# Kernel tuning notes

Measured on AMD Instinct MI355X. Metric: run time of the kernel, lower is better.

The kernel has to match this reference:

```python
import jax, jax.numpy as jnp
import numpy as np

N = 32          # objects in the (single) image
P = N * (N - 1) # relation pairs
D = 256         # self.dim
M = 14          # mask_size / pooler resolution
OC = 151        # obj classes
RC = 51         # rel classes
RED = D // 4    # attention gate reduction


def setup_inputs() -> dict:
    key = jax.random.key(0)
    ks = jax.random.split(key, 32)
    # all ordered pairs i != j
    ii, jj = np.meshgrid(np.arange(N), np.arange(N), indexing='ij')
    keep = ii != jj
    rel_pair_idxs = jnp.asarray(np.stack([ii[keep], jj[keep]], 1), jnp.int32)  # [P,2]
    # valid xyxy boxes in an 800x600 image
    x1 = jax.random.uniform(ks[0], (N,)) * 600.0
    y1 = jax.random.uniform(ks[1], (N,)) * 400.0
    w = jax.random.uniform(ks[2], (N,)) * 180.0 + 20.0
    h = jax.random.uniform(ks[3], (N,)) * 180.0 + 20.0
    bboxes = jnp.stack([x1, y1, x1 + w, y1 + h], 1).astype(jnp.float32)
    roi_features = jax.random.normal(ks[4], (N, 4096), jnp.float32)
    predict_logits = jax.random.normal(ks[5], (N, OC), jnp.float32)
    union_features = jax.random.normal(ks[6], (P, D, M, M), jnp.float32)
    s = 0.02
    p = dict(
        roi_features=roi_features, bboxes=bboxes, predict_logits=predict_logits,
        union_features=union_features, rel_pair_idxs=rel_pair_idxs,
        W_emb1=jax.random.normal(ks[7], (4096 + OC + 4, D)) * s, b_emb1=jnp.zeros((D,)),
        W_emb2=jax.random.normal(ks[8], (D, D)) * s, b_emb2=jnp.zeros((D,)),
        # stacked SE-attention gates: 0=sbj, 1=obj, 2=bg
        att_fc1_w=jax.random.normal(ks[9], (3, D, RED)) * s, att_fc1_b=jnp.zeros((3, RED)),
        att_fc2_w=jax.random.normal(ks[10], (3, RED, D)) * s, att_fc2_b=jnp.zeros((3, D)),
        W_c1=jax.random.normal(ks[11], (3 * D, D)) * s, b_c1=jnp.zeros((D,)),
        W_c2=jax.random.normal(ks[12], (D, D)) * s, b_c2=jnp.zeros((D,)),
        W_gcn=jax.random.normal(ks[13], (D, D)) * s, b_gcn=jnp.zeros((D,)),
        W_objp=jax.random.normal(ks[14], (D, OC)) * s, b_objp=jnp.zeros((OC,)),
        W_relp=jax.random.normal(ks[15], (D, RC)) * s, b_relp=jnp.zeros((RC,)),
    )
    return p


def _rect_masks(x0, y0, x1, y1):
    # mask[p, r, c] = 1 iff x0<=r<x1 and y0<=c<y1  (matches torch slice write)
    r = jnp.arange(M, dtype=jnp.float32)
    rm = (r[None, :] >= x0[:, None]) & (r[None, :] < x1[:, None])  # [P,M]
    cm = (r[None, :] >= y0[:, None]) & (r[None, :] < y1[:, None])  # [P,M]
    return (rm[:, :, None] & cm[:, None, :]).astype(jnp.float32)   # [P,M,M]


def _masking(union_features, bboxes, pairs):
    sb = bboxes[pairs[:, 0]]  # [P,4]
    ob = bboxes[pairs[:, 1]]
    ux1 = jnp.minimum(sb[:, 0], ob[:, 0])
    uy1 = jnp.minimum(sb[:, 1], ob[:, 1])
    x = jnp.stack([sb[:, 0], sb[:, 2], ob[:, 0], ob[:, 2]], 1) - ux1[:, None]
    y = jnp.stack([sb[:, 1], sb[:, 3], ob[:, 1], ob[:, 3]], 1) - uy1[:, None]
    xr = M / jnp.maximum(x[:, 1], x[:, 3])
    yr = M / jnp.maximum(y[:, 1], y[:, 3])
    xp = jnp.round(x * xr[:, None])
    yp = jnp.round(y * yr[:, None])
    sm = _rect_masks(xp[:, 0], yp[:, 0], xp[:, 1], yp[:, 1])[:, None]  # [P,1,M,M]
    om = _rect_masks(xp[:, 2], yp[:, 2], xp[:, 3], yp[:, 3])[:, None]
    bm = jnp.clip(1.0 - sm - om, 0.0, 1.0)
    return union_features * sm, union_features * om, union_features * bm


def _att_gate(x, w1, b1, w2, b2):
    # SE-style channel attention gate
    s = x.mean((2, 3))                                        # [P,D]
    g = jax.nn.sigmoid(jax.nn.relu(s @ w1 + b1) @ w2 + b2)    # [P,D]
    return x * g[:, :, None, None]


def _adjacency(pairs):
    o2o = jnp.zeros((N, N)).at[pairs[:, 0], pairs[:, 1]].set(1.0)
    ar = jnp.arange(P)
    o2r = jnp.zeros((N, P)).at[pairs[:, 0], ar].set(1.0).at[pairs[:, 1], ar].set(1.0)
    top = jnp.concatenate([o2o, o2r], 1)                     # [N, N+P]
    bot = jnp.concatenate([o2r.T, jnp.zeros((P, P))], 1)     # [P, N+P]
    adj = jnp.concatenate([top, bot], 0)
    return adj + jnp.eye(N + P)


def reference(roi_features, bboxes, predict_logits, union_features, rel_pair_idxs,
              W_emb1, b_emb1, W_emb2, b_emb2,
              att_fc1_w, att_fc1_b, att_fc2_w, att_fc2_b,
              W_c1, b_c1, W_c2, b_c2, W_gcn, b_gcn,
              W_objp, b_objp, W_relp, b_relp):
    pairs = rel_pair_idxs
    # object embedding
    obj_in = jnp.concatenate([roi_features, predict_logits, bboxes], 1)  # [N,4251]
    obj_feats = jax.nn.relu(obj_in @ W_emb1 + b_emb1) @ W_emb2 + b_emb2  # [N,D]
    # masking + attention gates + global avg pool
    sbj, obj, bg = _masking(union_features, bboxes, pairs)
    sbj = _att_gate(sbj, att_fc1_w[0], att_fc1_b[0], att_fc2_w[0], att_fc2_b[0]).mean((2, 3))
    obj = _att_gate(obj, att_fc1_w[1], att_fc1_b[1], att_fc2_w[1], att_fc2_b[1]).mean((2, 3))
    bg = _att_gate(bg, att_fc1_w[2], att_fc1_b[2], att_fc2_w[2], att_fc2_b[2]).mean((2, 3))
    # relational embedding (compose)
    rel = jnp.concatenate([sbj, obj, bg], 1)                 # [P,3D]
    rel_feats = jax.nn.relu(rel @ W_c1 + b_c1) @ W_c2 + b_c2  # [P,D]
    # GCN over object+relation graph (row-normalized adjacency, residual)
    adj = _adjacency(pairs)
    feats = jnp.concatenate([obj_feats, rel_feats], 0)        # [N+P,D]
    norm_adj = adj / adj.sum(1, keepdims=True)
    gcn_out = jax.nn.relu(norm_adj @ (feats @ W_gcn) + b_gcn) + feats
    obj_dists = gcn_out[:N] @ W_objp + b_objp                 # [N,OC]
    rel_dists = gcn_out[N:] @ W_relp + b_relp                 # [P,RC]
    return obj_dists, rel_dists
```

## Files before the change

kernel.cpp:

```cpp
#include <hip/hip_runtime.h>
#include <cstdint>
#include <cstddef>

#define NOBJ 32
#define NP   992
#define DD   256
#define SP   196
#define OC   151
#define RC   51
#define RED  64
#define KIN  4251
#define CH   128
#define KPC  34

#define OFF_PART   0u
#define OFF_OBJF   1048576u
#define OFF_SALL   1056768u
#define OFF_RELF   1818624u
#define OFF_H      2072576u
#define OFF_WOPT   2826240u
#define OFF_WRPT   2864896u

#define TR_TOT 51712

#define TCH  32
#define NTIL 8
#define TF4  1568

__global__ void __launch_bounds__(256, 5)
k_pre(const float* __restrict__ uf,
      const float* __restrict__ bbox,
      const int* __restrict__ pairs,
      const float* __restrict__ roi,
      const float* __restrict__ logits,
      const float* __restrict__ W1,
      const float* __restrict__ Wop, const float* __restrict__ Wrp,
      float* __restrict__ sAll, float* __restrict__ part,
      float* __restrict__ WopT, float* __restrict__ WrpT) {
  const int b = blockIdx.x, t = threadIdx.x;
  if (b < NP) {
    const int p = b;
    __shared__ __align__(16) float buf[TCH * SP + 28];
    __shared__ __align__(16) float mS[224];
    __shared__ __align__(16) float mO[224];
    __shared__ __align__(16) float mB[224];
    if (t < 224) {
      float sm = 0.f, om = 0.f, bm = 0.f;
      if (t < SP) {
        int si = pairs[2 * p], oi = pairs[2 * p + 1];
        float sx1 = bbox[si * 4 + 0], sy1 = bbox[si * 4 + 1];
        float sx2 = bbox[si * 4 + 2], sy2 = bbox[si * 4 + 3];
        float ox1 = bbox[oi * 4 + 0], oy1 = bbox[oi * 4 + 1];
        float ox2 = bbox[oi * 4 + 2], oy2 = bbox[oi * 4 + 3];
        float ux = fminf(sx1, ox1), uy = fminf(sy1, oy1);
        float xr = 14.f / fmaxf(sx2 - ux, ox2 - ux);
        float yr = 14.f / fmaxf(sy2 - uy, oy2 - uy);
        float xs0 = rintf((sx1 - ux) * xr), xs1 = rintf((sx2 - ux) * xr);
        float xo0 = rintf((ox1 - ux) * xr), xo1 = rintf((ox2 - ux) * xr);
        float ys0 = rintf((sy1 - uy) * yr), ys1 = rintf((sy2 - uy) * yr);
        float yo0 = rintf((oy1 - uy) * yr), yo1 = rintf((oy2 - uy) * yr);
        int a = t / 14, bb = t - a * 14;
        float fa = (float)a, fb = (float)bb;
        sm = (fa >= xs0 && fa < xs1 && fb >= ys0 && fb < ys1) ? 1.f : 0.f;
        om = (fa >= xo0 && fa < xo1 && fb >= yo0 && fb < yo1) ? 1.f : 0.f;
        bm = fminf(fmaxf(1.f - sm - om, 0.f), 1.f);
      }
      mS[t] = sm; mO[t] = om; mB[t] = bm;
    }
    if (t < 28) buf[TCH * SP + t] = 0.f;
    const float4* base4 = (const float4*)(uf + (size_t)p * (DD * SP));
    {
      const float4* src = base4 + t;
      float4* dst = (float4*)buf + t;
      dst[0] = src[0];     dst[256] = src[256];   dst[512] = src[512];
      dst[768] = src[768]; dst[1024] = src[1024]; dst[1280] = src[1280];
      if (t < 32) dst[1536] = src[1536];
    }
    __syncthreads();
    const int cl = t >> 3, o = t & 7;
    const float* row = buf + cl * SP + o * 28;
    const float* msp = mS + o * 28;
    const float* mop = mO + o * 28;
    const float* mbp = mB + o * 28;
    const float inv = 1.f / 196.f;
    float4 s0, s1, s2, s3, s4, s5, s6 = {0.f, 0.f, 0.f, 0.f};
#pragma unroll 1
    for (int ti = 0; ti < NTIL; ++ti) {
      if (ti < NTIL - 1) {
        const float4* src = base4 + (ti + 1) * TF4 + t;
        s0 = src[0];     s1 = src[256];   s2 = src[512];
        s3 = src[768];   s4 = src[1024];  s5 = src[1280];
        if (t < 32) s6 = src[1536];
      }
      float aS = 0.f, aO = 0.f, aB = 0.f;
#pragma unroll
      for (int j = 0; j < 7; ++j) {
        float4 v = *(const float4*)&row[4 * j];
        float4 x = *(const float4*)&msp[4 * j];
        float4 y = *(const float4*)&mop[4 * j];
        float4 z = *(const float4*)&mbp[4 * j];
        aS += v.x * x.x + v.y * x.y + v.z * x.z + v.w * x.w;
        aO += v.x * y.x + v.y * y.y + v.z * y.z + v.w * y.w;
        aB += v.x * z.x + v.y * z.y + v.z * z.z + v.w * z.w;
      }
      aS += __shfl_xor(aS, 1); aS += __shfl_xor(aS, 2); aS += __shfl_xor(aS, 4);
      aO += __shfl_xor(aO, 1); aO += __shfl_xor(aO, 2); aO += __shfl_xor(aO, 4);
      aB += __shfl_xor(aB, 1); aB += __shfl_xor(aB, 2); aB += __shfl_xor(aB, 4);
      const int ch = ti * TCH + cl;
      if (o == 0)      sAll[(size_t)p * 768 + ch]       = aS * inv;
      else if (o == 1) sAll[(size_t)p * 768 + 256 + ch] = aO * inv;
      else if (o == 2) sAll[(size_t)p * 768 + 512 + ch] = aB * inv;
      if (ti < NTIL - 1) {
        __syncthreads();
        float4* dst = (float4*)buf + t;
        dst[0] = s0;     dst[256] = s1;   dst[512] = s2;
        dst[768] = s3;   dst[1024] = s4;  dst[1280] = s5;
        if (t < 32) dst[1536] = s6;
        __syncthreads();
      }
    }
  } else if (b < NP + CH) {
    const int chunk = b - NP;
    int k0 = chunk * KPC;
    int k1 = k0 + KPC; if (k1 > KIN) k1 = KIN;
    float acc[NOBJ];
#pragma unroll
    for (int i = 0; i < NOBJ; ++i) acc[i] = 0.f;
#pragma unroll 2
    for (int k = k0; k < k1; ++k) {
      float w = W1[(size_t)k * DD + t];
      const float* xp; int stride;
      if (k < 4096)            { xp = roi    + k;               stride = 4096; }
      else if (k < 4096 + OC)  { xp = logits + (k - 4096);      stride = OC;   }
      else                     { xp = bbox   + (k - 4096 - OC); stride = 4;    }
#pragma unroll
      for (int i = 0; i < NOBJ; ++i) { acc[i] += xp[0] * w; xp += stride; }
    }
    float* pout = part + (size_t)chunk * (NOBJ * DD) + t;
#pragma unroll
    for (int i = 0; i < NOBJ; ++i) pout[i * DD] = acc[i];
  } else {
    for (int o = (b - NP - CH) * 256 + t; o < TR_TOT; o += 64 * 256) {
      float v; float* dst;
      if (o < 38656) { int q = o;         v = Wop[(q & 255) * OC + (q >> 8)]; dst = WopT + q; }
      else           { int q = o - 38656; v = Wrp[(q & 255) * RC + (q >> 8)]; dst = WrpT + q; }
      *dst = v;
    }
  }
}

#define DOT8(WP, STR, X0, X1, K, A0, A1)                                      \
  { float w0v = (WP)[(size_t)((K) + 0) * (STR)],                              \
          w1v = (WP)[(size_t)((K) + 1) * (STR)],                              \
          w2v = (WP)[(size_t)((K) + 2) * (STR)],                              \
          w3v = (WP)[(size_t)((K) + 3) * (STR)],                              \
          w4v = (WP)[(size_t)((K) + 4) * (STR)],                              \
          w5v = (WP)[(size_t)((K) + 5) * (STR)],                              \
          w6v = (WP)[(size_t)((K) + 6) * (STR)],                              \
          w7v = (WP)[(size_t)((K) + 7) * (STR)];                              \
    float4 xa0 = *(const float4*)&(X0)[(K)];                                  \
    float4 xb0 = *(const float4*)&(X0)[(K) + 4];                              \
    float4 xa1 = *(const float4*)&(X1)[(K)];                                  \
    float4 xb1 = *(const float4*)&(X1)[(K) + 4];                              \
    A0 += xa0.x * w0v + xa0.y * w1v + xa0.z * w2v + xa0.w * w3v               \
        + xb0.x * w4v + xb0.y * w5v + xb0.z * w6v + xb0.w * w7v;              \
    A1 += xa1.x * w0v + xa1.y * w1v + xa1.z * w2v + xa1.w * w3v               \
        + xb1.x * w4v + xb1.y * w5v + xb1.z * w6v + xb1.w * w7v; }

__global__ void __launch_bounds__(256, 4)
k_mid2(const float* __restrict__ sAll,
       const float* __restrict__ f1w, const float* __restrict__ f1b,
       const float* __restrict__ f2w, const float* __restrict__ f2b,
       const float* __restrict__ Wc1, const float* __restrict__ bc1,
       const float* __restrict__ Wc2, const float* __restrict__ bc2,
       const float* __restrict__ Wg,
       const float* __restrict__ part, const float* __restrict__ b1,
       const float* __restrict__ W2,  const float* __restrict__ b2,
       float* __restrict__ relf, float* __restrict__ objf,
       float* __restrict__ H) {
  const int b = blockIdx.x, t = threadIdx.x;
  __shared__ __align__(16) float sg[2][768];
  __shared__ __align__(16) float ha[2][192];
  __shared__ __align__(16) float h2[2][256];
  __shared__ __align__(16) float rf[2][256];
  __shared__ __align__(16) float hob[256];
  __shared__ __align__(16) float eob[256];
  if (b < NP / 2) {
    const int r0 = b * 2;
    const int tt = t;
    for (int j = t; j < 384; j += 256) {
      int pr = j / 192, off = j - pr * 192;
      ((float4*)&sg[pr][0])[off] =
          ((const float4*)(sAll + (size_t)(r0 + pr) * 768))[off];
    }
    __syncthreads();
    if (tt < 192) {
      const int br = tt >> 6;
      const float* wp = f1w + br * 16384 + (tt & 63);
      const float* x0 = &sg[0][br * 256];
      const float* x1 = &sg[1][br * 256];
      float a0 = 0.f, a1 = 0.f;
      for (int k8 = 0; k8 < 32; ++k8) DOT8(wp, 64, x0, x1, k8 * 8, a0, a1)
      float bb = f1b[tt];
      ha[0][tt] = fmaxf(a0 + bb, 0.f);
      ha[1][tt] = fmaxf(a1 + bb, 0.f);
    }
    __syncthreads();
#pragma unroll
    for (int br = 0; br < 3; ++br) {
      const float* wp = f2w + br * 16384 + tt;
      const float* x0 = &ha[0][br * 64];
      const float* x1 = &ha[1][br * 64];
      float a0 = 0.f, a1 = 0.f;
      for (int r8 = 0; r8 < 8; ++r8) DOT8(wp, 256, x0, x1, r8 * 8, a0, a1)
      float bb = f2b[br * 256 + tt];
      sg[0][br * 256 + tt] *= 1.f / (1.f + expf(-(a0 + bb)));
      sg[1][br * 256 + tt] *= 1.f / (1.f + expf(-(a1 + bb)));
    }
    __syncthreads();
    {
      const float* wp = Wc1 + tt;
      const float* x0 = &sg[0][0];
      const float* x1 = &sg[1][0];
      float a0 = 0.f, a1 = 0.f;
      for (int k8 = 0; k8 < 96; ++k8) DOT8(wp, 256, x0, x1, k8 * 8, a0, a1)
      float bb = bc1[tt];
      h2[0][tt] = fmaxf(a0 + bb, 0.f);
      h2[1][tt] = fmaxf(a1 + bb, 0.f);
    }
    __syncthreads();
    {
      const float* wp = Wc2 + tt;
      const float* x0 = &h2[0][0];
      const float* x1 = &h2[1][0];
      float a0 = 0.f, a1 = 0.f;
      for (int k8 = 0; k8 < 32; ++k8) DOT8(wp, 256, x0, x1, k8 * 8, a0, a1)
      float bb = bc2[tt];
      float v0 = a0 + bb, v1 = a1 + bb;
      relf[(size_t)r0 * DD + tt] = v0;
      relf[(size_t)(r0 + 1) * DD + tt] = v1;
      rf[0][tt] = v0; rf[1][tt] = v1;
    }
    __syncthreads();
    {
      const float* wp = Wg + tt;
      const float* x0 = &rf[0][0];
      const float* x1 = &rf[1][0];
      float a0 = 0.f, a1 = 0.f;
      for (int k8 = 0; k8 < 32; ++k8) DOT8(wp, 256, x0, x1, k8 * 8, a0, a1)
      H[(size_t)(NOBJ + r0) * DD + tt] = a0;
      H[(size_t)(NOBJ + r0 + 1) * DD + tt] = a1;
    }
  } else {
    const int i = b - NP / 2;
    float s[8];
#pragma unroll
    for (int u = 0; u < 8; ++u) s[u] = 0.f;
#pragma unroll
    for (int c0 = 0; c0 < CH; c0 += 8) {
#pragma unroll
      for (int u = 0; u < 8; ++u)
        s[u] += part[(size_t)(c0 + u) * (NOBJ * DD) + i * DD + t];
    }
    float tot = ((s[0] + s[1]) + (s[2] + s[3])) + ((s[4] + s[5]) + (s[6] + s[7]));
    hob[t] = fmaxf(tot + b1[t], 0.f);
    __syncthreads();
    {
      float a = 0.f;
#pragma unroll 4
      for (int k4 = 0; k4 < 64; ++k4) {
        float4 hv = *((const float4*)hob + k4);
        int k = 4 * k4;
        a += hv.x * W2[k * 256 + t]       + hv.y * W2[(k + 1) * 256 + t]
           + hv.z * W2[(k + 2) * 256 + t] + hv.w * W2[(k + 3) * 256 + t];
      }
      float v = a + b2[t];
      objf[i * DD + t] = v;
      eob[t] = v;
    }
    __syncthreads();
    {
      float a = 0.f;
#pragma unroll 4
      for (int k4 = 0; k4 < 64; ++k4) {
        float4 ev = *((const float4*)eob + k4);
        int k = 4 * k4;
        a += ev.x * Wg[k * 256 + t]       + ev.y * Wg[(k + 1) * 256 + t]
           + ev.z * Wg[(k + 2) * 256 + t] + ev.w * Wg[(k + 3) * 256 + t];
      }
      H[(size_t)i * DD + t] = a;
    }
  }
}

__global__ void __launch_bounds__(1024, 1)
k_heads(const float* __restrict__ H, const float* __restrict__ objf,
        const float* __restrict__ relf, const int* __restrict__ pairs,
        const float* __restrict__ bg,
        const float* __restrict__ WopT, const float* __restrict__ bop,
        const float* __restrict__ WrpT, const float* __restrict__ brp,
        float* __restrict__ out) {
  const int b = blockIdx.x, t = threadIdx.x;
  const int p = t >> 8, tt = t & 255;
  if (b < NP / 4) {
    __shared__ __align__(16) float gr[4][DD];
    __shared__ float red[4][4][64];
    const int r = b * 4 + p;
    int si = pairs[2 * r], oi = pairs[2 * r + 1];
    float hsum = H[si * DD + tt] + H[oi * DD + tt] + H[(size_t)(NOBJ + r) * DD + tt];
    gr[p][tt] = fmaxf(hsum * (1.f / 3.f) + bg[tt], 0.f) + relf[(size_t)r * DD + tt];
    __syncthreads();
    const int q = tt >> 6, c = tt & 63;
    float a = 0.f;
    if (c < RC) {
      const float4* w4 = (const float4*)(WrpT + c * 256 + q * 64);
#pragma unroll
      for (int j = 0; j < 16; ++j) {
        float4 wv = w4[j];
        float4 gv = *(const float4*)&gr[p][q * 64 + 4 * j];
        a += gv.x * wv.x + gv.y * wv.y + gv.z * wv.z + gv.w * wv.w;
      }
    }
    red[p][q][c] = a;
    __syncthreads();
    if (tt < RC)
      out[NOBJ * OC + (size_t)r * RC + tt] =
          red[p][0][tt] + red[p][1][tt] + red[p][2][tt] + red[p][3][tt] + brp[tt];
  } else {
    const int i = b - NP / 4;
    const int slice = p;
    __shared__ int2 pr[NP];
    __shared__ float red2[4][DD];
    __shared__ __align__(16) float gro[DD];
    const int2* p2 = (const int2*)pairs;
    for (int r = t; r < NP; r += 1024) pr[r] = p2[r];
    __syncthreads();
    float acc = 0.f;
    if (slice == 0) {
#pragma unroll 8
      for (int j = 0; j < NOBJ; ++j) acc += H[j * DD + tt];
    }
    const int rbeg = slice * 248;
#pragma unroll 8
    for (int r = rbeg; r < rbeg + 248; ++r) {
      int2 q = pr[r];
      float v = H[(size_t)(NOBJ + r) * DD + tt];
      if (q.x == i || q.y == i) acc += v;
    }
    red2[slice][tt] = acc;
    __syncthreads();
    if (t < DD) {
      float pre = (red2[0][t] + red2[1][t] + red2[2][t] + red2[3][t]) * (1.f / 94.f);
      gro[t] = fmaxf(pre + bg[t], 0.f) + objf[i * DD + t];
    }
    __syncthreads();
    float hsum = 0.f;
    if (tt < OC) {
      const float4* w4 = (const float4*)(WopT + tt * 256 + slice * 64);
#pragma unroll
      for (int j = 0; j < 16; ++j) {
        float4 wv = w4[j];
        float4 gv = *(const float4*)&gro[slice * 64 + 4 * j];
        hsum += gv.x * wv.x + gv.y * wv.y + gv.z * wv.z + gv.w * wv.w;
      }
    }
    red2[slice][tt] = hsum;
    __syncthreads();
    if (t < OC)
      out[i * OC + t] = red2[0][t] + red2[1][t] + red2[2][t] + red2[3][t] + bop[t];
  }
}

extern "C" void kernel_launch(void* const* d_in, const int* in_sizes, int n_in,
                              void* d_out, int out_size, void* d_ws, size_t ws_size,
                              hipStream_t stream) {
  const float* roi   = (const float*)d_in[0];
  const float* bbox  = (const float*)d_in[1];
  const float* logit = (const float*)d_in[2];
  const float* uf    = (const float*)d_in[3];
  const int*   pairs = (const int*)d_in[4];
  const float* W1    = (const float*)d_in[5];
  const float* b1    = (const float*)d_in[6];
  const float* W2    = (const float*)d_in[7];
  const float* b2    = (const float*)d_in[8];
  const float* fc1w  = (const float*)d_in[9];
  const float* fc1b  = (const float*)d_in[10];
  const float* fc2w  = (const float*)d_in[11];
  const float* fc2b  = (const float*)d_in[12];
  const float* Wc1   = (const float*)d_in[13];
  const float* bc1   = (const float*)d_in[14];
  const float* Wc2   = (const float*)d_in[15];
  const float* bc2   = (const float*)d_in[16];
  const float* Wg    = (const float*)d_in[17];
  const float* bg    = (const float*)d_in[18];
  const float* Wop   = (const float*)d_in[19];
  const float* bop   = (const float*)d_in[20];
  const float* Wrp   = (const float*)d_in[21];
  const float* brp   = (const float*)d_in[22];

  float* ws    = (float*)d_ws;
  float* part  = ws + OFF_PART;
  float* objf  = ws + OFF_OBJF;
  float* sAll  = ws + OFF_SALL;
  float* relf  = ws + OFF_RELF;
  float* Hbuf  = ws + OFF_H;
  float* WopT  = ws + OFF_WOPT;
  float* WrpT  = ws + OFF_WRPT;
  float* out   = (float*)d_out;

  k_pre<<<NP + CH + 64, 256, 0, stream>>>(uf, bbox, pairs, roi, logit, W1,
                                          Wop, Wrp, sAll, part, WopT, WrpT);
  k_mid2<<<NP / 2 + NOBJ, 256, 0, stream>>>(sAll, fc1w, fc1b, fc2w, fc2b,
                                            Wc1, bc1, Wc2, bc2, Wg,
                                            part, b1, W2, b2, relf, objf, Hbuf);
  k_heads<<<NP / 4 + NOBJ, 1024, 0, stream>>>(Hbuf, objf, relf, pairs, bg,
                                              WopT, bop, WrpT, brp, out);
}
```

Measured before the change: 454.5 us.

## Double-buffer union-feature tiles via direct global-to-LDS loads

The per-pair masking/pooling loop now streams each 32-channel tile straight from global memory into LDS with the global_load_lds builtin, using two LDS buffers so the next tile loads while the current one is reduced. This removes the register staging copy and one of the two barriers per tile. The cost is doubled LDS per block, so launch bounds drop from 5 to 3 blocks per CU. Correctness depends on the compiler inserting the right vmcnt waits before the barrier, since the builtin's completion is not otherwise awaited.

```diff
diff --git a/kernel.cpp b/kernel.cpp
--- a/kernel.cpp
+++ b/kernel.cpp
@@ -25,9 +25,27 @@
 
 #define TCH  32
 #define NTIL 8
-#define TF4  1568
-
-__global__ void __launch_bounds__(256, 5)
+#define TFLT 6272
+#define BUFSZ 6304
+
+#if defined(__has_builtin)
+#if __has_builtin(__builtin_amdgcn_global_load_lds)
+#define HAS_GLLDS 1
+#endif
+#endif
+
+__device__ __forceinline__ void gl_lds16(const float* g, float* l) {
+#ifdef HAS_GLLDS
+  __builtin_amdgcn_global_load_lds(
+      (const __attribute__((address_space(1))) void*)g,
+      (__attribute__((address_space(3))) void*)l,
+      16, 0, 0);
+#else
+  *(float4*)l = *(const float4*)g;
+#endif
+}
+
+__global__ void __launch_bounds__(256, 3)
 k_pre(const float* __restrict__ uf,
       const float* __restrict__ bbox,
       const int* __restrict__ pairs,
@@ -40,7 +58,7 @@
   const int b = blockIdx.x, t = threadIdx.x;
   if (b < NP) {
     const int p = b;
-    __shared__ __align__(16) float buf[TCH * SP + 28];
+    __shared__ __align__(16) float buf[2][BUFSZ];
     __shared__ __align__(16) float mS[224];
     __shared__ __align__(16) float mO[224];
     __shared__ __align__(16) float mB[224];
@@ -67,31 +85,27 @@
       }
       mS[t] = sm; mO[t] = om; mB[t] = bm;
     }
-    if (t < 28) buf[TCH * SP + t] = 0.f;
-    const float4* base4 = (const float4*)(uf + (size_t)p * (DD * SP));
-    {
-      const float4* src = base4 + t;
-      float4* dst = (float4*)buf + t;
-      dst[0] = src[0];     dst[256] = src[256];   dst[512] = src[512];
-      dst[768] = src[768]; dst[1024] = src[1024]; dst[1280] = src[1280];
-      if (t < 32) dst[1536] = src[1536];
-    }
+    if (t < 28) { buf[0][TFLT + t] = 0.f; buf[1][TFLT + t] = 0.f; }
+    const float* gbase = uf + (size_t)p * (DD * SP);
+#define ISSUE_TILE(TI, BI)                                                    \
+    { const float* src = gbase + (TI) * TFLT + t * 4;                         \
+      float* dst = &buf[BI][t * 4];                                           \
+      gl_lds16(src, dst);                 gl_lds16(src + 1024, dst + 1024);   \
+      gl_lds16(src + 2048, dst + 2048);   gl_lds16(src + 3072, dst + 3072);   \
+      gl_lds16(src + 4096, dst + 4096);   gl_lds16(src + 5120, dst + 5120);   \
+      if (t < 32) gl_lds16(src + 6144, dst + 6144); }
+    ISSUE_TILE(0, 0)
     __syncthreads();
     const int cl = t >> 3, o = t & 7;
-    const float* row = buf + cl * SP + o * 28;
+    const int roff = cl * SP + o * 28;
     const float* msp = mS + o * 28;
     const float* mop = mO + o * 28;
     const float* mbp = mB + o * 28;
     const float inv = 1.f / 196.f;
-    float4 s0, s1, s2, s3, s4, s5, s6 = {0.f, 0.f, 0.f, 0.f};
 #pragma unroll 1
     for (int ti = 0; ti < NTIL; ++ti) {
-      if (ti < NTIL - 1) {
-        const float4* src = base4 + (ti + 1) * TF4 + t;
-        s0 = src[0];     s1 = src[256];   s2 = src[512];
-        s3 = src[768];   s4 = src[1024];  s5 = src[1280];
-        if (t < 32) s6 = src[1536];
-      }
+      if (ti + 1 < NTIL) ISSUE_TILE(ti + 1, (ti + 1) & 1)
+      const float* row = &buf[ti & 1][roff];
       float aS = 0.f, aO = 0.f, aB = 0.f;
 #pragma unroll
       for (int j = 0; j < 7; ++j) {
@@ -110,15 +124,9 @@
       if (o == 0)      sAll[(size_t)p * 768 + ch]       = aS * inv;
       else if (o == 1) sAll[(size_t)p * 768 + 256 + ch] = aO * inv;
       else if (o == 2) sAll[(size_t)p * 768 + 512 + ch] = aB * inv;
-      if (ti < NTIL - 1) {
-        __syncthreads();
-        float4* dst = (float4*)buf + t;
-        dst[0] = s0;     dst[256] = s1;   dst[512] = s2;
-        dst[768] = s3;   dst[1024] = s4;  dst[1280] = s5;
-        if (t < 32) dst[1536] = s6;
-        __syncthreads();
-      }
-    }
+      __syncthreads();
+    }
+#undef ISSUE_TILE
   } else if (b < NP + CH) {
     const int chunk = b - NP;
     int k0 = chunk * KPC;
```

Result: no change. 456.9 us (+0.5%).
